# Kernel optimization log

Measured on AMD Instinct MI355X. Metric: run time of the kernel, lower is better.

The kernel has to match this reference:

```python
import jax, jax.numpy as jnp
import numpy as np

N = 50000
E = 1600000
D_IN = 256
HID = 64
HEADS = 4


def setup_inputs() -> dict:
    key = jax.random.key(0)
    ks = jax.random.split(key, 8)
    x = jax.random.normal(ks[0], (N, D_IN), dtype=jnp.float32)
    edge_index = jax.random.randint(ks[1], (2, E), 0, N, dtype=jnp.int32)
    # GATConv params (PyG default: concat=True, negative_slope=0.2, add_self_loops=True)
    W = jax.random.normal(ks[2], (D_IN, HEADS * HID), dtype=jnp.float32) * (1.0 / np.sqrt(D_IN))
    att_src = jax.random.normal(ks[3], (HEADS, HID), dtype=jnp.float32) * 0.1
    att_dst = jax.random.normal(ks[4], (HEADS, HID), dtype=jnp.float32) * 0.1
    bias = jnp.zeros((HEADS * HID,), dtype=jnp.float32)
    # fc1: Linear(hidden*4, 3)
    fc1_W = jax.random.normal(ks[5], (HEADS * HID, 3), dtype=jnp.float32) * (1.0 / np.sqrt(HEADS * HID))
    fc1_b = jnp.zeros((3,), dtype=jnp.float32)
    return {"x": x, "edge_index": edge_index, "W": W, "att_src": att_src,
            "att_dst": att_dst, "bias": bias, "fc1_W": fc1_W, "fc1_b": fc1_b}


def _gat_conv(x, edge_index, W, att_src, att_dst, bias):
    n = x.shape[0]
    xp = (x @ W).reshape(n, HEADS, HID)  # [N,H,C]
    # add self loops (PyG default)
    loops = jnp.arange(n, dtype=edge_index.dtype)
    src = jnp.concatenate([edge_index[0], loops])  # [E+N]
    dst = jnp.concatenate([edge_index[1], loops])
    a_src = jnp.sum(xp * att_src, axis=-1)  # [N,H]
    a_dst = jnp.sum(xp * att_dst, axis=-1)
    alpha = jax.nn.leaky_relu(a_src[src] + a_dst[dst], negative_slope=0.2)  # [E+N,H]
    # segment softmax over incoming edges of each dst node
    amax = jax.ops.segment_max(alpha, dst, num_segments=n)
    ex = jnp.exp(alpha - amax[dst])
    denom = jax.ops.segment_sum(ex, dst, num_segments=n)
    alpha = ex / (denom[dst] + 1e-16)
    msg = xp[src] * alpha[:, :, None]  # [E+N,H,C]
    out = jax.ops.segment_sum(msg, dst, num_segments=n)  # [N,H,C]
    return out.reshape(n, HEADS * HID) + bias


def reference(x, edge_index, W, att_src, att_dst, bias, fc1_W, fc1_b):
    # dropout is identity at inference
    h = _gat_conv(x, edge_index, W, att_src, att_dst, bias)
    h = jax.nn.leaky_relu(h, negative_slope=0.01)  # F.leaky_relu default slope
    edge_rep = h[edge_index[0]] * h[edge_index[1]] * 0.5  # [E, H*HID]
    edge_scores = edge_rep @ fc1_W + fc1_b  # [E, 3]
    return edge_scores
```

## Files before the change

kernel.cpp:

```cpp
#include <hip/hip_runtime.h>
#include <hip/hip_fp16.h>
#include <math.h>

constexpr int N    = 50000;
constexpr int E    = 1600000;
constexpr int F    = 256;
constexpr int EL   = E + N;
constexpr int NBLK = (N + 255) / 256;
constexpr int CH   = (EL + 15) / 16;

typedef _Float16 v8hf __attribute__((ext_vector_type(8)));
typedef float    v4f  __attribute__((ext_vector_type(4)));

__global__ __launch_bounds__(256) void k_prep(
    const float* __restrict__ W, const float* __restrict__ fc1W,
    _Float16* __restrict__ wt, _Float16* __restrict__ wt3h,
    int* __restrict__ counts) {
  const int t = blockIdx.x * 256 + threadIdx.x;
  {
    const int n = t >> 8, k = t & 255;
    wt[t] = (_Float16)W[k * 256 + n];
  }
  if (t < 4096) {
    const int n = t >> 8, k = t & 255;
    wt3h[t] = (n < 3) ? (_Float16)(0.5f * fc1W[k * 3 + n]) : (_Float16)0.f;
  }
  if (t < N) counts[t] = 0;
}

__global__ __launch_bounds__(256) void k_xw_mfma(
    const float* __restrict__ x, const _Float16* __restrict__ wt,
    const float* __restrict__ att_src, const float* __restrict__ att_dst,
    const int* __restrict__ ei, int* __restrict__ counts,
    __half* __restrict__ xp, float* __restrict__ a_src, float* __restrict__ a_dst) {
  const int wv   = threadIdx.x >> 6;
  const int lane = threadIdx.x & 63;
  const int q = lane >> 4, l16 = lane & 15;
  const int m0 = blockIdx.x * 16;
  const int c0 = wv * 64;

  v4f acc[4] = {{0,0,0,0},{0,0,0,0},{0,0,0,0},{0,0,0,0}};
  const float*    arow = x  + (size_t)(m0 + l16) * 256 + q * 8;
  const _Float16* brow = wt + (size_t)(c0 + l16) * 256 + q * 8;

  for (int kc = 0; kc < 256; kc += 32) {
    const float4 f0 = *(const float4*)(arow + kc);
    const float4 f1 = *(const float4*)(arow + kc + 4);
    const v8hf a = {(_Float16)f0.x, (_Float16)f0.y, (_Float16)f0.z, (_Float16)f0.w,
                    (_Float16)f1.x, (_Float16)f1.y, (_Float16)f1.z, (_Float16)f1.w};
    #pragma unroll
    for (int tn = 0; tn < 4; ++tn) {
      const v8hf b = *(const v8hf*)(brow + (size_t)tn * 16 * 256 + kc);
      acc[tn] = __builtin_amdgcn_mfma_f32_16x16x32_f16(a, b, acc[tn], 0, 0, 0);
    }
  }

  #pragma unroll
  for (int tn = 0; tn < 4; ++tn) {
    const int col = c0 + tn * 16 + l16;
    #pragma unroll
    for (int r = 0; r < 4; ++r)
      xp[(size_t)(m0 + q * 4 + r) * 256 + col] = __float2half_rn(acc[tn][r]);
  }

  float aw[4], dw[4];
  #pragma unroll
  for (int tn = 0; tn < 4; ++tn) {
    aw[tn] = att_src[c0 + tn * 16 + l16];
    dw[tn] = att_dst[c0 + tn * 16 + l16];
  }
  #pragma unroll
  for (int r = 0; r < 4; ++r) {
    float ps = acc[0][r]*aw[0] + acc[1][r]*aw[1] + acc[2][r]*aw[2] + acc[3][r]*aw[3];
    float pd = acc[0][r]*dw[0] + acc[1][r]*dw[1] + acc[2][r]*dw[2] + acc[3][r]*dw[3];
    #pragma unroll
    for (int off = 1; off < 16; off <<= 1) {
      ps += __shfl_xor(ps, off, 16);
      pd += __shfl_xor(pd, off, 16);
    }
    if (l16 == 0) {
      a_src[(m0 + q * 4 + r) * 4 + wv] = ps;
      a_dst[(m0 + q * 4 + r) * 4 + wv] = pd;
    }
  }

  const int gid = blockIdx.x * 256 + threadIdx.x;
  for (int i = gid; i < E; i += 800000) atomicAdd(&counts[ei[E + i]], 1);
}

__global__ __launch_bounds__(256) void k_scan1(
    const int* __restrict__ counts, int* __restrict__ offsets, int* __restrict__ partials) {
  __shared__ int s[256];
  const int t = threadIdx.x;
  const int i = blockIdx.x * 256 + t;
  const int v = (i < N) ? counts[i] + 1 : 0;
  s[t] = v;
  __syncthreads();
  for (int off = 1; off < 256; off <<= 1) {
    const int add = (t >= off) ? s[t - off] : 0;
    __syncthreads();
    s[t] += add;
    __syncthreads();
  }
  if (i < N) offsets[i] = s[t] - v;
  if (t == 255) partials[blockIdx.x] = s[255];
}

__global__ __launch_bounds__(256) void k_scan3b(
    int* __restrict__ offsets, const int* __restrict__ partials,
    int* __restrict__ cursor) {
  __shared__ int s[256];
  const int t = threadIdx.x, b = blockIdx.x;
  const int v = (t < NBLK) ? partials[t] : 0;
  s[t] = v;
  __syncthreads();
  for (int off = 1; off < 256; off <<= 1) {
    const int add = (t >= off) ? s[t - off] : 0;
    __syncthreads();
    s[t] += add;
    __syncthreads();
  }
  const int pre = (b == 0) ? 0 : s[b - 1];
  const int i = b * 256 + t;
  if (i < N) {
    const int val = offsets[i] + pre;
    offsets[i] = val;
    cursor[i]  = val;
  }
  if (i == 0) offsets[N] = EL;
}

__global__ void k_scatter(const int* __restrict__ ei, int* __restrict__ cursor,
                          int4* __restrict__ se) {
  const int i = blockIdx.x * blockDim.x + threadIdx.x;
  if (i >= EL) return;
  int s, d, id;
  if (i < E) { s = ei[i]; d = ei[E + i]; id = i; }
  else       { s = d = i - E; id = -1; }
  const int pos = atomicAdd(&cursor[d], 1);
  se[pos] = make_int4(s, id, d, 0);
}

__global__ __launch_bounds__(128) void k_agg(
    const __half* __restrict__ xp, const float* __restrict__ a_src,
    const float* __restrict__ a_dst, const int4* __restrict__ se,
    const int* __restrict__ offsets, const float* __restrict__ bias,
    __half* __restrict__ h) {
  const int n = blockIdx.x;
  const int t = threadIdx.x;
  const int wv = t >> 6, lane = t & 63;
  const int hd = lane >> 4, es = lane & 15;
  const int beg = offsets[n], end = offsets[n + 1];
  const float adst = a_dst[n * 4 + hd];
  const __half* xb = xp + (size_t)lane * 4;

  float a0 = 0.f, a1 = 0.f, a2 = 0.f, a3 = 0.f, den = 0.f;

  for (int c = beg + wv * 16; c < end; c += 32) {
    const int cnt = min(16, end - c);
    int sv = 0; float wvv = 0.f;
    if (es < cnt) {
      sv = se[c + es].x;
      float al = a_src[sv * 4 + hd] + adst;
      al = al > 0.f ? al : 0.2f * al;
      wvv = __expf(al);
    }
    if (cnt == 16) {
      #pragma unroll
      for (int g = 0; g < 2; ++g) {
        int ss[8]; float ww[8]; uint2 rr[8];
        #pragma unroll
        for (int j = 0; j < 8; ++j) {
          ss[j] = __shfl(sv,  g * 8 + j, 16);
          ww[j] = __shfl(wvv, g * 8 + j, 16);
        }
        #pragma unroll
        for (int j = 0; j < 8; ++j) rr[j] = *(const uint2*)(xb + (size_t)ss[j] * 256);
        #pragma unroll
        for (int j = 0; j < 8; ++j) {
          const __half2* p = (const __half2*)&rr[j];
          const float2 lo = __half22float2(p[0]), hi = __half22float2(p[1]);
          den += ww[j];
          a0 += ww[j] * lo.x; a1 += ww[j] * lo.y;
          a2 += ww[j] * hi.x; a3 += ww[j] * hi.y;
        }
      }
    } else {
      for (int j = 0; j < cnt; ++j) {
        const int   s = __shfl(sv, j, 16);
        const float w = __shfl(wvv, j, 16);
        const uint2 r = *(const uint2*)(xb + (size_t)s * 256);
        const __half2* p = (const __half2*)&r;
        const float2 lo = __half22float2(p[0]), hi = __half22float2(p[1]);
        den += w;
        a0 += w * lo.x; a1 += w * lo.y; a2 += w * hi.x; a3 += w * hi.y;
      }
    }
  }

  __shared__ float ra[256];
  __shared__ float rd[64];
  if (wv == 1) {
    ra[lane * 4 + 0] = a0; ra[lane * 4 + 1] = a1;
    ra[lane * 4 + 2] = a2; ra[lane * 4 + 3] = a3;
    rd[lane] = den;
  }
  __syncthreads();
  if (wv == 0) {
    a0 += ra[lane * 4 + 0]; a1 += ra[lane * 4 + 1];
    a2 += ra[lane * 4 + 2]; a3 += ra[lane * 4 + 3];
    den += rd[lane];
    const float inv = 1.f / (den + 1e-16f);
    const float4 bv = *(const float4*)(bias + lane * 4);
    float o0 = a0 * inv + bv.x, o1 = a1 * inv + bv.y;
    float o2 = a2 * inv + bv.z, o3 = a3 * inv + bv.w;
    o0 = o0 > 0.f ? o0 : 0.01f * o0;
    o1 = o1 > 0.f ? o1 : 0.01f * o1;
    o2 = o2 > 0.f ? o2 : 0.01f * o2;
    o3 = o3 > 0.f ? o3 : 0.01f * o3;
    const __half2 p0 = __floats2half2_rn(o0, o1), p1 = __floats2half2_rn(o2, o3);
    uint2 st;
    st.x = *(const unsigned*)&p0;
    st.y = *(const unsigned*)&p1;
    *(uint2*)(h + (size_t)n * 256 + lane * 4) = st;
  }
}

__global__ __launch_bounds__(256) void k_score_flat(
    const _Float16* __restrict__ h, const int4* __restrict__ se,
    const _Float16* __restrict__ wt3h, const float* __restrict__ fc1b,
    float* __restrict__ out, int total_waves) {
  const int lane = threadIdx.x & 63;
  const int q = lane >> 4, l16 = lane & 15;
  const int wgid = blockIdx.x * 4 + (threadIdx.x >> 6);

  v8hf bfrag[8];
  {
    const _Float16* brow = wt3h + l16 * 256 + q * 8;
    #pragma unroll
    for (int kci = 0; kci < 8; ++kci) bfrag[kci] = *(const v8hf*)(brow + kci * 32);
  }
  const float bn = (l16 < 3) ? fc1b[l16] : 0.f;

  for (int ch = wgid; ch < CH; ch += total_waves) {
    const int idx = ch * 16 + l16;
    int s = 0, d = 0, eid = -1;
    if (idx < EL) { const int4 p = se[idx]; s = p.x; eid = p.y; d = p.z; }

    const _Float16* srow = h + (size_t)s * 256 + q * 8;
    const _Float16* drow = h + (size_t)d * 256 + q * 8;
    v8hf av[8], dv[8];
    #pragma unroll
    for (int kci = 0; kci < 8; ++kci) av[kci] = *(const v8hf*)(srow + kci * 32);
    #pragma unroll
    for (int kci = 0; kci < 8; ++kci) dv[kci] = *(const v8hf*)(drow + kci * 32);

    v4f acc = {0.f, 0.f, 0.f, 0.f};
    #pragma unroll
    for (int kci = 0; kci < 8; ++kci) {
      const v8hf ar = av[kci] * dv[kci];
      acc = __builtin_amdgcn_mfma_f32_16x16x32_f16(ar, bfrag[kci], acc, 0, 0, 0);
    }

    #pragma unroll
    for (int r = 0; r < 4; ++r) {
      const int m = q * 4 + r;
      const int em = __shfl(eid, m, 16);
      if (l16 < 3 && em >= 0)
        out[(size_t)em * 3 + l16] = acc[r] + bn;
    }
  }
}

static inline size_t align256(size_t b) { return (b + 255) & ~(size_t)255; }

extern "C" void kernel_launch(void* const* d_in, const int* in_sizes, int n_in,
                              void* d_out, int out_size, void* d_ws, size_t ws_size,
                              hipStream_t stream) {
  const float* x    = (const float*)d_in[0];
  const int*   ei   = (const int*)  d_in[1];
  const float* W    = (const float*)d_in[2];
  const float* attS = (const float*)d_in[3];
  const float* attD = (const float*)d_in[4];
  const float* bias = (const float*)d_in[5];
  const float* fc1W = (const float*)d_in[6];
  const float* fc1b = (const float*)d_in[7];
  float*       out  = (float*)d_out;
  char*        ws   = (char*)d_ws;

  size_t off = 0;
  auto alloc = [&](size_t bytes) -> void* {
    void* p = ws + off;
    off += align256(bytes);
    return p;
  };
  _Float16* wt     = (_Float16*)alloc((size_t)F * F * sizeof(_Float16));
  _Float16* wt3h   = (_Float16*)alloc((size_t)16 * F * sizeof(_Float16));
  __half*   xp     = (__half*)  alloc((size_t)N * F * sizeof(__half));
  __half*   hbuf   = (__half*)  alloc((size_t)N * F * sizeof(__half));
  float*    a_src  = (float*)   alloc((size_t)N * 4 * sizeof(float));
  float*    a_dst  = (float*)   alloc((size_t)N * 4 * sizeof(float));
  int*      counts = (int*)     alloc((size_t)N * sizeof(int));
  int*      offs   = (int*)     alloc((size_t)(N + 1) * sizeof(int));
  int*      partial= (int*)     alloc(256 * sizeof(int));
  int*      cursor = (int*)     alloc((size_t)N * sizeof(int));
  int4*     se     = (int4*)    alloc((size_t)EL * sizeof(int4));

  k_prep<<<256, 256, 0, stream>>>(W, fc1W, wt, wt3h, counts);
  k_xw_mfma<<<N / 16, 256, 0, stream>>>(x, wt, attS, attD, ei, counts,
                                        xp, a_src, a_dst);
  k_scan1<<<NBLK, 256, 0, stream>>>(counts, offs, partial);
  k_scan3b<<<NBLK, 256, 0, stream>>>(offs, partial, cursor);
  k_scatter<<<(EL + 255) / 256, 256, 0, stream>>>(ei, cursor, se);
  k_agg<<<N, 128, 0, stream>>>(xp, a_src, a_dst, se, offs, bias, hbuf);
  const int score_blocks = 4096;
  k_score_flat<<<score_blocks, 256, 0, stream>>>((const _Float16*)hbuf, se, wt3h,
                                                 fc1b, out, score_blocks * 4);
}
```

Baseline: 594.7 us.

## Fuse CSR build stages into one cooperative kernel with grid syncs

```diff
diff --git a/kernel.cpp b/kernel.cpp
--- a/kernel.cpp
+++ b/kernel.cpp
@@ -1,6 +1,9 @@
 #include <hip/hip_runtime.h>
 #include <hip/hip_fp16.h>
+#include <hip/hip_cooperative_groups.h>
 #include <math.h>
+
+namespace cg = cooperative_groups;
 
 constexpr int N    = 50000;
 constexpr int E    = 1600000;
@@ -12,88 +15,33 @@
 typedef _Float16 v8hf __attribute__((ext_vector_type(8)));
 typedef float    v4f  __attribute__((ext_vector_type(4)));
 
-__global__ __launch_bounds__(256) void k_prep(
-    const float* __restrict__ W, const float* __restrict__ fc1W,
-    _Float16* __restrict__ wt, _Float16* __restrict__ wt3h,
-    int* __restrict__ counts) {
-  const int t = blockIdx.x * 256 + threadIdx.x;
-  {
-    const int n = t >> 8, k = t & 255;
-    wt[t] = (_Float16)W[k * 256 + n];
-  }
-  if (t < 4096) {
-    const int n = t >> 8, k = t & 255;
-    wt3h[t] = (n < 3) ? (_Float16)(0.5f * fc1W[k * 3 + n]) : (_Float16)0.f;
-  }
-  if (t < N) counts[t] = 0;
-}
-
-__global__ __launch_bounds__(256) void k_xw_mfma(
-    const float* __restrict__ x, const _Float16* __restrict__ wt,
-    const float* __restrict__ att_src, const float* __restrict__ att_dst,
-    const int* __restrict__ ei, int* __restrict__ counts,
-    __half* __restrict__ xp, float* __restrict__ a_src, float* __restrict__ a_dst) {
-  const int wv   = threadIdx.x >> 6;
-  const int lane = threadIdx.x & 63;
-  const int q = lane >> 4, l16 = lane & 15;
-  const int m0 = blockIdx.x * 16;
-  const int c0 = wv * 64;
-
-  v4f acc[4] = {{0,0,0,0},{0,0,0,0},{0,0,0,0},{0,0,0,0}};
-  const float*    arow = x  + (size_t)(m0 + l16) * 256 + q * 8;
-  const _Float16* brow = wt + (size_t)(c0 + l16) * 256 + q * 8;
-
-  for (int kc = 0; kc < 256; kc += 32) {
-    const float4 f0 = *(const float4*)(arow + kc);
-    const float4 f1 = *(const float4*)(arow + kc + 4);
-    const v8hf a = {(_Float16)f0.x, (_Float16)f0.y, (_Float16)f0.z, (_Float16)f0.w,
-                    (_Float16)f1.x, (_Float16)f1.y, (_Float16)f1.z, (_Float16)f1.w};
-    #pragma unroll
-    for (int tn = 0; tn < 4; ++tn) {
-      const v8hf b = *(const v8hf*)(brow + (size_t)tn * 16 * 256 + kc);
-      acc[tn] = __builtin_amdgcn_mfma_f32_16x16x32_f16(a, b, acc[tn], 0, 0, 0);
-    }
-  }
-
-  #pragma unroll
-  for (int tn = 0; tn < 4; ++tn) {
-    const int col = c0 + tn * 16 + l16;
-    #pragma unroll
-    for (int r = 0; r < 4; ++r)
-      xp[(size_t)(m0 + q * 4 + r) * 256 + col] = __float2half_rn(acc[tn][r]);
-  }
-
-  float aw[4], dw[4];
-  #pragma unroll
-  for (int tn = 0; tn < 4; ++tn) {
-    aw[tn] = att_src[c0 + tn * 16 + l16];
-    dw[tn] = att_dst[c0 + tn * 16 + l16];
-  }
-  #pragma unroll
-  for (int r = 0; r < 4; ++r) {
-    float ps = acc[0][r]*aw[0] + acc[1][r]*aw[1] + acc[2][r]*aw[2] + acc[3][r]*aw[3];
-    float pd = acc[0][r]*dw[0] + acc[1][r]*dw[1] + acc[2][r]*dw[2] + acc[3][r]*dw[3];
-    #pragma unroll
-    for (int off = 1; off < 16; off <<= 1) {
-      ps += __shfl_xor(ps, off, 16);
-      pd += __shfl_xor(pd, off, 16);
-    }
-    if (l16 == 0) {
-      a_src[(m0 + q * 4 + r) * 4 + wv] = ps;
-      a_dst[(m0 + q * 4 + r) * 4 + wv] = pd;
-    }
-  }
-
-  const int gid = blockIdx.x * 256 + threadIdx.x;
-  for (int i = gid; i < E; i += 800000) atomicAdd(&counts[ei[E + i]], 1);
-}
-
-__global__ __launch_bounds__(256) void k_scan1(
-    const int* __restrict__ counts, int* __restrict__ offsets, int* __restrict__ partials) {
+__global__ __launch_bounds__(256) void k_csr(
+    const int* __restrict__ ei, const float* __restrict__ W,
+    const float* __restrict__ fc1W, _Float16* __restrict__ wt,
+    _Float16* __restrict__ wt3h, int* __restrict__ counts,
+    int* __restrict__ offsets, int* __restrict__ partials,
+    int* __restrict__ cursor, int4* __restrict__ se) {
+  cg::grid_group grid = cg::this_grid();
+  const int t = threadIdx.x, b = blockIdx.x;
+  const int gid = b * 256 + t;
+  constexpr int GT = NBLK * 256;
+
+  for (int i = gid; i < F * F; i += GT) {
+    const int n = i >> 8, k = i & 255;
+    wt[i] = (_Float16)W[k * 256 + n];
+  }
+  if (gid < 4096) {
+    const int n = gid >> 8, k = gid & 255;
+    wt3h[gid] = (n < 3) ? (_Float16)(0.5f * fc1W[k * 3 + n]) : (_Float16)0.f;
+  }
+  if (gid < N) counts[gid] = 0;
+  grid.sync();
+
+  for (int i = gid; i < E; i += GT) atomicAdd(&counts[ei[E + i]], 1);
+  grid.sync();
+
   __shared__ int s[256];
-  const int t = threadIdx.x;
-  const int i = blockIdx.x * 256 + t;
-  const int v = (i < N) ? counts[i] + 1 : 0;
+  const int v = (gid < N) ? counts[gid] + 1 : 0;
   s[t] = v;
   __syncthreads();
   for (int off = 1; off < 256; off <<= 1) {
@@ -102,43 +50,94 @@
     s[t] += add;
     __syncthreads();
   }
-  if (i < N) offsets[i] = s[t] - v;
-  if (t == 255) partials[blockIdx.x] = s[255];
-}
-
-__global__ __launch_bounds__(256) void k_scan3b(
-    int* __restrict__ offsets, const int* __restrict__ partials,
-    int* __restrict__ cursor) {
-  __shared__ int s[256];
-  const int t = threadIdx.x, b = blockIdx.x;
-  const int v = (t < NBLK) ? partials[t] : 0;
-  s[t] = v;
-  __syncthreads();
-  for (int off = 1; off < 256; off <<= 1) {
-    const int add = (t >= off) ? s[t - off] : 0;
+  if (gid < N) offsets[gid] = s[t] - v;
+  if (t == 255) partials[b] = s[255];
+  grid.sync();
+
+  {
+    const int pv = (t < NBLK) ? partials[t] : 0;
     __syncthreads();
-    s[t] += add;
+    s[t] = pv;
     __syncthreads();
-  }
-  const int pre = (b == 0) ? 0 : s[b - 1];
-  const int i = b * 256 + t;
-  if (i < N) {
-    const int val = offsets[i] + pre;
-    offsets[i] = val;
-    cursor[i]  = val;
-  }
-  if (i == 0) offsets[N] = EL;
-}
-
-__global__ void k_scatter(const int* __restrict__ ei, int* __restrict__ cursor,
-                          int4* __restrict__ se) {
-  const int i = blockIdx.x * blockDim.x + threadIdx.x;
-  if (i >= EL) return;
-  int s, d, id;
-  if (i < E) { s = ei[i]; d = ei[E + i]; id = i; }
-  else       { s = d = i - E; id = -1; }
-  const int pos = atomicAdd(&cursor[d], 1);
-  se[pos] = make_int4(s, id, d, 0);
+    for (int off = 1; off < 256; off <<= 1) {
+      const int add = (t >= off) ? s[t - off] : 0;
+      __syncthreads();
+      s[t] += add;
+      __syncthreads();
+    }
+    const int pre = (b == 0) ? 0 : s[b - 1];
+    if (gid < N) {
+      const int val = offsets[gid] + pre;
+      offsets[gid] = val;
+      cursor[gid]  = val;
+    }
+    if (gid == 0) offsets[N] = EL;
+  }
+  grid.sync();
+
+  for (int i = gid; i < EL; i += GT) {
+    int sn, d, id;
+    if (i < E) { sn = ei[i]; d = ei[E + i]; id = i; }
+    else       { sn = d = i - E; id = -1; }
+    const int pos = atomicAdd(&cursor[d], 1);
+    se[pos] = make_int4(sn, id, d, 0);
+  }
+}
+
+__global__ __launch_bounds__(256) void k_xw_mfma(
+    const float* __restrict__ x, const _Float16* __restrict__ wt,
+    const float* __restrict__ att_src, const float* __restrict__ att_dst,
+    __half* __restrict__ xp, float* __restrict__ a_src, float* __restrict__ a_dst) {
+  const int wv   = threadIdx.x >> 6;
+  const int lane = threadIdx.x & 63;
+  const int q = lane >> 4, l16 = lane & 15;
+  const int m0 = blockIdx.x * 16;
+  const int c0 = wv * 64;
+
+  v4f acc[4] = {{0,0,0,0},{0,0,0,0},{0,0,0,0},{0,0,0,0}};
+  const float*    arow = x  + (size_t)(m0 + l16) * 256 + q * 8;
+  const _Float16* brow = wt + (size_t)(c0 + l16) * 256 + q * 8;
+
+  for (int kc = 0; kc < 256; kc += 32) {
+    const float4 f0 = *(const float4*)(arow + kc);
+    const float4 f1 = *(const float4*)(arow + kc + 4);
+    const v8hf a = {(_Float16)f0.x, (_Float16)f0.y, (_Float16)f0.z, (_Float16)f0.w,
+                    (_Float16)f1.x, (_Float16)f1.y, (_Float16)f1.z, (_Float16)f1.w};
+    #pragma unroll
+    for (int tn = 0; tn < 4; ++tn) {
+      const v8hf bfr = *(const v8hf*)(brow + (size_t)tn * 16 * 256 + kc);
+      acc[tn] = __builtin_amdgcn_mfma_f32_16x16x32_f16(a, bfr, acc[tn], 0, 0, 0);
+    }
+  }
+
+  #pragma unroll
+  for (int tn = 0; tn < 4; ++tn) {
+    const int col = c0 + tn * 16 + l16;
+    #pragma unroll
+    for (int r = 0; r < 4; ++r)
+      xp[(size_t)(m0 + q * 4 + r) * 256 + col] = __float2half_rn(acc[tn][r]);
+  }
+
+  float aw[4], dw[4];
+  #pragma unroll
+  for (int tn = 0; tn < 4; ++tn) {
+    aw[tn] = att_src[c0 + tn * 16 + l16];
+    dw[tn] = att_dst[c0 + tn * 16 + l16];
+  }
+  #pragma unroll
+  for (int r = 0; r < 4; ++r) {
+    float ps = acc[0][r]*aw[0] + acc[1][r]*aw[1] + acc[2][r]*aw[2] + acc[3][r]*aw[3];
+    float pd = acc[0][r]*dw[0] + acc[1][r]*dw[1] + acc[2][r]*dw[2] + acc[3][r]*dw[3];
+    #pragma unroll
+    for (int off = 1; off < 16; off <<= 1) {
+      ps += __shfl_xor(ps, off, 16);
+      pd += __shfl_xor(pd, off, 16);
+    }
+    if (l16 == 0) {
+      a_src[(m0 + q * 4 + r) * 4 + wv] = ps;
+      a_dst[(m0 + q * 4 + r) * 4 + wv] = pd;
+    }
+  }
 }
 
 __global__ __launch_bounds__(128) void k_agg(
@@ -306,12 +305,14 @@
   int*      cursor = (int*)     alloc((size_t)N * sizeof(int));
   int4*     se     = (int4*)    alloc((size_t)EL * sizeof(int4));
 
-  k_prep<<<256, 256, 0, stream>>>(W, fc1W, wt, wt3h, counts);
-  k_xw_mfma<<<N / 16, 256, 0, stream>>>(x, wt, attS, attD, ei, counts,
-                                        xp, a_src, a_dst);
-  k_scan1<<<NBLK, 256, 0, stream>>>(counts, offs, partial);
-  k_scan3b<<<NBLK, 256, 0, stream>>>(offs, partial, cursor);
-  k_scatter<<<(EL + 255) / 256, 256, 0, stream>>>(ei, cursor, se);
+  {
+    void* args[] = {(void*)&ei, (void*)&W, (void*)&fc1W, (void*)&wt, (void*)&wt3h,
+                    (void*)&counts, (void*)&offs, (void*)&partial, (void*)&cursor,
+                    (void*)&se};
+    hipLaunchCooperativeKernel((const void*)k_csr, dim3(NBLK), dim3(256),
+                               args, 0, stream);
+  }
+  k_xw_mfma<<<N / 16, 256, 0, stream>>>(x, wt, attS, attD, xp, a_src, a_dst);
   k_agg<<<N, 128, 0, stream>>>(xp, a_src, a_dst, se, offs, bias, hbuf);
   const int score_blocks = 4096;
   k_score_flat<<<score_blocks, 256, 0, stream>>>((const _Float16*)hbuf, se, wt3h,
```

Result: slower. 685.4 us (+15.3%).
